# Performance work log

Hardware: AMD Instinct MI355X
Metric: run time of the kernel (lower is better)

Reference implementation:

```python
import jax, jax.numpy as jnp
import numpy as np

NUM_EXPERTS = 8
NUM_LANGS = 4
TOP_K = 2
D_MODEL = 1024
EXPERT_SIZE = 4096
B, S = 2, 2048


def setup_inputs() -> dict:
    key = jax.random.key(0)
    ks = jax.random.split(key, 6)
    def xavier(k, shape, fan_in, fan_out):
        a = float(np.sqrt(6.0 / (fan_in + fan_out)))
        return jax.random.uniform(k, shape, jnp.float32, -a, a)
    return {
        "x": jax.random.normal(ks[0], (B, S, D_MODEL), jnp.float32),
        "router_w": xavier(ks[1], (NUM_EXPERTS, D_MODEL), D_MODEL, NUM_EXPERTS),
        "router_b": jnp.zeros((NUM_EXPERTS,), jnp.float32),
        "lang_w": xavier(ks[2], (NUM_LANGS, D_MODEL), D_MODEL, NUM_LANGS),
        "lang_b": jnp.zeros((NUM_LANGS,), jnp.float32),
        "w1": xavier(ks[3], (NUM_EXPERTS, D_MODEL, EXPERT_SIZE), D_MODEL, EXPERT_SIZE),
        "b1": jnp.zeros((NUM_EXPERTS, EXPERT_SIZE), jnp.float32),
        "w2": xavier(ks[4], (NUM_EXPERTS, EXPERT_SIZE, D_MODEL), EXPERT_SIZE, D_MODEL),
        "b2": jnp.zeros((NUM_EXPERTS, D_MODEL), jnp.float32),
    }


def reference(x, router_w, router_b, lang_w, lang_b, w1, b1, w2, b2):
    # Language-aware routing bias
    lang_logits = x @ lang_w.T + lang_b                      # [B,S,L]
    lang_probs = jax.nn.softmax(lang_logits, axis=-1)
    # lang_probs[..., idx:idx+2].sum(-1): slice may be width 1 at the edge,
    # emulate with a zero pad column.
    lp_pad = jnp.pad(lang_probs, ((0, 0), (0, 0), (0, 1)))
    idx = jnp.arange(NUM_EXPERTS) % NUM_LANGS                # [E]
    expert_weights = lp_pad[..., idx] + lp_pad[..., idx + 1] # [B,S,E]

    router_logits = x @ router_w.T + router_b + 0.1 * expert_weights
    router_probs = jax.nn.softmax(router_logits, axis=-1)   # [B,S,E]
    top_p, top_i = jax.lax.top_k(router_probs, TOP_K)        # [B,S,K]
    top_p = top_p / top_p.sum(axis=-1, keepdims=True)

    # Dense per-expert MLP (dropout=0 / eval). torch GELU default = exact erf.
    h = jax.nn.gelu(jnp.einsum('bsd,edh->bseh', x, w1) + b1, approximate=False)
    expert_out = jnp.einsum('bseh,ehd->bsed', h, w2) + b2    # [B,S,E,D]

    sel = jnp.take_along_axis(expert_out, top_i[..., None], axis=2)  # [B,S,K,D]
    return (top_p[..., None] * sel).sum(axis=2)              # [B,S,D]
```

## Files before the change

### kernel.cpp

```cpp
#include <hip/hip_runtime.h>
#include <cstdint>
#include <cstddef>

#define T_TOK 4096
#define DM 1024
#define HS 4096
#define NE 8
#define MAXROWS 9216
#define MAXTILES 72

typedef __attribute__((ext_vector_type(8))) short short8;
typedef __attribute__((ext_vector_type(4))) float floatx4;

__device__ __forceinline__ unsigned short f2bf(float f) {
  union { float f; unsigned u; } v; v.f = f;
  unsigned r = (v.u + 0x7fffu + ((v.u >> 16) & 1u)) >> 16;
  return (unsigned short)r;
}

__device__ __forceinline__ void gload_lds16(const void* g, void* l) {
  __builtin_amdgcn_global_load_lds((const __attribute__((address_space(1))) void*)g,
                                   (__attribute__((address_space(3))) void*)l, 16, 0, 0);
}


__global__ void k_init(int* counts, int* cursor, unsigned* list) {
  int i = blockIdx.x * 256 + threadIdx.x;
  if (i < NE) { counts[i] = 0; cursor[i] = 0; }
  if (i < MAXROWS) list[i] = 0xFFFFFFFFu;
}

__global__ void k_route(const float* __restrict__ x, const float* __restrict__ rw,
                        const float* __restrict__ rb, const float* __restrict__ lw,
                        const float* __restrict__ lb, int* __restrict__ top_i,
                        float* __restrict__ top_p, int* __restrict__ counts) {
  int t = blockIdx.x * 4 + (threadIdx.x >> 6);
  int lane = threadIdx.x & 63;
  const float4* xt = (const float4*)(x + (size_t)t * DM);
  float4 xv[4];
#pragma unroll
  for (int j = 0; j < 4; j++) xv[j] = xt[lane * 4 + j];
  float dots[12];
#pragma unroll
  for (int r = 0; r < 12; r++) {
    const float4* wr = (const float4*)(r < 4 ? lw + r * DM : rw + (r - 4) * DM);
    float s = 0.f;
#pragma unroll
    for (int j = 0; j < 4; j++) {
      float4 w = wr[lane * 4 + j];
      s += xv[j].x * w.x + xv[j].y * w.y + xv[j].z * w.z + xv[j].w * w.w;
    }
#pragma unroll
    for (int o = 32; o > 0; o >>= 1) s += __shfl_xor(s, o, 64);
    dots[r] = s;
  }
  if (lane == 0) {
    float lp[4]; float m = -1e30f;
#pragma unroll
    for (int i = 0; i < 4; i++) { lp[i] = dots[i] + lb[i]; m = fmaxf(m, lp[i]); }
    float sum = 0.f;
#pragma unroll
    for (int i = 0; i < 4; i++) { lp[i] = expf(lp[i] - m); sum += lp[i]; }
#pragma unroll
    for (int i = 0; i < 4; i++) lp[i] /= sum;
    float ew[4];
    ew[0] = lp[0] + lp[1]; ew[1] = lp[1] + lp[2]; ew[2] = lp[2] + lp[3]; ew[3] = lp[3];
    float r8[8];
#pragma unroll
    for (int e = 0; e < 8; e++) r8[e] = dots[4 + e] + rb[e] + 0.1f * ew[e & 3];
    int e0 = 0;
#pragma unroll
    for (int e = 1; e < 8; e++) if (r8[e] > r8[e0]) e0 = e;
    int e1 = (e0 == 0) ? 1 : 0;
#pragma unroll
    for (int e = 0; e < 8; e++) if (e != e0 && r8[e] > r8[e1]) e1 = e;
    float tt = expf(r8[e1] - r8[e0]);
    float w0 = 1.f / (1.f + tt);
    float w1 = tt / (1.f + tt);
    top_i[t * 2] = e0; top_i[t * 2 + 1] = e1;
    top_p[t * 2] = w0; top_p[t * 2 + 1] = w1;
    atomicAdd(&counts[e0], 1); atomicAdd(&counts[e1], 1);
  }
}

__global__ void k_offsets(const int* counts, int* off) {
  if (threadIdx.x == 0) {
    int acc = 0;
    for (int e = 0; e < NE; e++) {
      off[e] = acc;
      int p = ((counts[e] + 127) >> 7) << 7;
      acc += p;
    }
    off[NE] = acc;
  }
}

__global__ void k_scatter(const int* __restrict__ top_i, const int* __restrict__ off,
                          int* cursor, unsigned* __restrict__ list) {
  int t = blockIdx.x * 256 + threadIdx.x;
  if (t >= T_TOK) return;
#pragma unroll
  for (int k = 0; k < 2; k++) {
    int e = top_i[t * 2 + k];
    int pos = atomicAdd(&cursor[e], 1);
    list[off[e] + pos] = (unsigned)(t * 2 + k);
  }
}

__global__ void k_cvt_x(const float* __restrict__ x, unsigned short* __restrict__ xb) {
  int i = blockIdx.x * 256 + threadIdx.x;
  float4 v = ((const float4*)x)[i];
  union { unsigned short us[4]; uint2 u2; } o;
  o.us[0] = f2bf(v.x); o.us[1] = f2bf(v.y); o.us[2] = f2bf(v.z); o.us[3] = f2bf(v.w);
  ((uint2*)xb)[i] = o.u2;
}

__global__ void k_transpose_bf16(const float* __restrict__ src, unsigned short* __restrict__ dst,
                                 int K, int N) {
  __shared__ float tile[64][65];
  const float* s = src + (size_t)blockIdx.z * K * N;
  unsigned short* d = dst + (size_t)blockIdx.z * K * N;
  int n0 = blockIdx.x * 64, k0 = blockIdx.y * 64;
  int r = threadIdx.x >> 6, c = threadIdx.x & 63;
#pragma unroll
  for (int j = 0; j < 16; j++) tile[r + j * 4][c] = s[(size_t)(k0 + r + j * 4) * N + n0 + c];
  __syncthreads();
#pragma unroll
  for (int j = 0; j < 16; j++) d[(size_t)(n0 + r + j * 4) * K + k0 + c] = f2bf(tile[c][r + j * 4]);
}

__global__ void k_init_out(const int* __restrict__ top_i, const float* __restrict__ top_p,
                           const float* __restrict__ b2, float* __restrict__ out) {
  int i = blockIdx.x * 256 + threadIdx.x;
  int t = i >> 10, d = i & 1023;
  int e0 = top_i[t * 2], e1 = top_i[t * 2 + 1];
  out[i] = top_p[t * 2] * b2[e0 * DM + d] + top_p[t * 2 + 1] * b2[e1 * DM + d];
}

template <int MODE>
__global__ __launch_bounds__(256, 2) void k_gemm(
    const unsigned short* __restrict__ Abase,
    const unsigned short* __restrict__ Wt,
    const int* __restrict__ off, const unsigned* __restrict__ list,
    const float* __restrict__ b1, const float* __restrict__ top_p,
    unsigned short* __restrict__ Hout, float* __restrict__ out,
    int K, int N) {
  int r0 = blockIdx.x * 128;
  int total = off[NE];
  if (r0 >= total) return;
  int e = 0;
  while (r0 >= off[e + 1]) ++e;
  int n0 = blockIdx.y * 128;

  __shared__ __align__(16) unsigned short lA[128 * 32];
  __shared__ __align__(16) unsigned short lB[128 * 32];
  __shared__ float sP[128];
  __shared__ int sTok[128];

  int tid = threadIdx.x;
  int srow = tid >> 2;
  int koff = (tid & 3) * 8;

  const unsigned short* srcA[2];
#pragma unroll
  for (int c = 0; c < 2; c++) {
    int row = c * 64 + srow;
    size_t arow;
    if (MODE == 0) {
      unsigned pair = list[r0 + row];
      arow = (pair == 0xFFFFFFFFu) ? 0 : (size_t)(pair >> 1);
    } else {
      arow = (size_t)(r0 + row);
    }
    srcA[c] = Abase + arow * K + koff;
  }
  const unsigned short* srcB[2];
#pragma unroll
  for (int c = 0; c < 2; c++)
    srcB[c] = Wt + ((size_t)e * N + n0 + c * 64 + srow) * K + koff;

  if (MODE == 1 && tid < 128) {
    unsigned pair = list[r0 + tid];
    if (pair == 0xFFFFFFFFu) { sTok[tid] = -1; sP[tid] = 0.f; }
    else { sTok[tid] = (int)(pair >> 1); sP[tid] = top_p[pair]; }
  }

  floatx4 acc[4][4] = {};
  int lane = tid & 63;
  int w = tid >> 6;
  int wm = w >> 1, wn = w & 1;
  int lr = lane & 15, kq = lane >> 4;
  const short8* pA = (const short8*)lA;
  const short8* pB = (const short8*)lB;

  for (int k0 = 0; k0 < K; k0 += 32) {
    __syncthreads();
#pragma unroll
    for (int c = 0; c < 2; c++) {
      gload_lds16(srcA[c] + k0, &lA[(c * 64 + srow) * 32 + koff]);
      gload_lds16(srcB[c] + k0, &lB[(c * 64 + srow) * 32 + koff]);
    }
    __syncthreads();
    short8 a[4], b[4];
#pragma unroll
    for (int i = 0; i < 4; i++) a[i] = pA[((wm * 64 + i * 16 + lr) * 32 + kq * 8) >> 3];
#pragma unroll
    for (int j = 0; j < 4; j++) b[j] = pB[((wn * 64 + j * 16 + lr) * 32 + kq * 8) >> 3];
#pragma unroll
    for (int i = 0; i < 4; i++)
#pragma unroll
      for (int j = 0; j < 4; j++)
        acc[i][j] = __builtin_amdgcn_mfma_f32_16x16x32_bf16(a[i], b[j], acc[i][j], 0, 0, 0);
  }

  int rbase = wm * 64 + kq * 4;
  int cbase = wn * 64 + lr;
  if (MODE == 0) {
#pragma unroll
    for (int i = 0; i < 4; i++)
#pragma unroll
      for (int j = 0; j < 4; j++)
#pragma unroll
        for (int g = 0; g < 4; g++) {
          int row = rbase + i * 16 + g;
          int col = cbase + j * 16;
          float v = acc[i][j][g] + b1[e * HS + n0 + col];
          v = 0.5f * v * (1.f + erff(v * 0.70710678118f));
          Hout[(size_t)(r0 + row) * (size_t)N + n0 + col] = f2bf(v);
        }
  } else {
#pragma unroll
    for (int i = 0; i < 4; i++)
#pragma unroll
      for (int j = 0; j < 4; j++)
#pragma unroll
        for (int g = 0; g < 4; g++) {
          int row = rbase + i * 16 + g;
          int col = cbase + j * 16;
          int tok = sTok[row];
          if (tok >= 0)
            atomicAdd(&out[(size_t)tok * DM + n0 + col], sP[row] * acc[i][j][g]);
        }
  }
}


extern "C" void kernel_launch(void* const* d_in, const int* in_sizes, int n_in,
                              void* d_out, int out_size, void* d_ws, size_t ws_size,
                              hipStream_t stream) {
  const float* x  = (const float*)d_in[0];
  const float* rw = (const float*)d_in[1];
  const float* rb = (const float*)d_in[2];
  const float* lw = (const float*)d_in[3];
  const float* lb = (const float*)d_in[4];
  const float* w1 = (const float*)d_in[5];
  const float* b1 = (const float*)d_in[6];
  const float* w2 = (const float*)d_in[7];
  const float* b2 = (const float*)d_in[8];
  float* out = (float*)d_out;
  char* ws = (char*)d_ws;

  int* counts = (int*)ws;
  int* cursor = (int*)(ws + 32);
  int* off    = (int*)(ws + 64);
  int* top_i  = (int*)(ws + 128);
  float* top_p = (float*)(ws + 128 + 32768);
  unsigned* list = (unsigned*)(ws + 65792);
  unsigned short* xb = (unsigned short*)(ws + 102912);
  unsigned short* wt = (unsigned short*)(ws + 102912 + 8388608);
  unsigned short* h  = (unsigned short*)(ws + 102912 + 8388608 + 67108864);

  k_init<<<dim3((MAXROWS + 255) / 256), dim3(256), 0, stream>>>(counts, cursor, list);
  k_route<<<dim3(T_TOK / 4), dim3(256), 0, stream>>>(x, rw, rb, lw, lb, top_i, top_p, counts);
  k_offsets<<<dim3(1), dim3(64), 0, stream>>>(counts, off);
  k_scatter<<<dim3(T_TOK / 256), dim3(256), 0, stream>>>(top_i, off, cursor, list);
  k_cvt_x<<<dim3(T_TOK * DM / 4 / 256), dim3(256), 0, stream>>>(x, xb);
  k_transpose_bf16<<<dim3(HS / 64, DM / 64, NE), dim3(256), 0, stream>>>(w1, wt, DM, HS);
  k_gemm<0><<<dim3(MAXTILES, HS / 128), dim3(256), 0, stream>>>(
      xb, wt, off, list, b1, top_p, h, nullptr, DM, HS);
  k_transpose_bf16<<<dim3(DM / 64, HS / 64, NE), dim3(256), 0, stream>>>(w2, wt, HS, DM);
  k_init_out<<<dim3(T_TOK * DM / 256), dim3(256), 0, stream>>>(top_i, top_p, b2, out);
  k_gemm<1><<<dim3(MAXTILES, DM / 128), dim3(256), 0, stream>>>(
      h, wt, off, list, nullptr, top_p, nullptr, out, HS, DM);
}
```

Before: 533.9 us.

## Double-buffer GEMM LDS loads, swizzle LDS layout, remap tiles, vectorize transpose

The GEMM main loop now double-buffers its LDS tiles, issuing the next k-slice load before running the MFMAs on the current one, and needs one barrier per iteration instead of two. The global-to-LDS source offsets are XOR-swizzled by row so that fragment reads avoid LDS bank conflicts. Block indices are remapped with a stride-8 interleave, presumably to spread tiles across XCDs or improve L2 reuse, and the grid is transposed to match. Occupancy hint is raised to 4 blocks per CU. The weight transpose kernel now uses float4 reads and 8-byte bf16 writes. The costs are twice the LDS, added register pressure, and a swizzle formula that assumes the tile count divides by 8.

Measured after the change: 515.4 us. 1.04x faster.

```diff
diff --git a/kernel.cpp b/kernel.cpp
--- a/kernel.cpp
+++ b/kernel.cpp
@@ -121,12 +121,24 @@
   const float* s = src + (size_t)blockIdx.z * K * N;
   unsigned short* d = dst + (size_t)blockIdx.z * K * N;
   int n0 = blockIdx.x * 64, k0 = blockIdx.y * 64;
-  int r = threadIdx.x >> 6, c = threadIdx.x & 63;
-#pragma unroll
-  for (int j = 0; j < 16; j++) tile[r + j * 4][c] = s[(size_t)(k0 + r + j * 4) * N + n0 + c];
+  int tr = threadIdx.x >> 4;
+  int tc = (threadIdx.x & 15) * 4;
+#pragma unroll
+  for (int j = 0; j < 4; j++) {
+    int row = tr + j * 16;
+    float4 v = *(const float4*)&s[(size_t)(k0 + row) * N + n0 + tc];
+    tile[row][tc + 0] = v.x; tile[row][tc + 1] = v.y;
+    tile[row][tc + 2] = v.z; tile[row][tc + 3] = v.w;
+  }
   __syncthreads();
 #pragma unroll
-  for (int j = 0; j < 16; j++) d[(size_t)(n0 + r + j * 4) * K + k0 + c] = f2bf(tile[c][r + j * 4]);
+  for (int j = 0; j < 4; j++) {
+    int n = tr + j * 16;
+    union { unsigned short us[4]; uint2 u2; } o;
+#pragma unroll
+    for (int i = 0; i < 4; i++) o.us[i] = f2bf(tile[tc + i][n]);
+    *(uint2*)&d[(size_t)(n0 + n) * K + k0 + tc] = o.u2;
+  }
 }
 
 __global__ void k_init_out(const int* __restrict__ top_i, const float* __restrict__ top_p,
@@ -138,28 +150,35 @@
 }
 
 template <int MODE>
-__global__ __launch_bounds__(256, 2) void k_gemm(
+__global__ __launch_bounds__(256, 4) void k_gemm(
     const unsigned short* __restrict__ Abase,
     const unsigned short* __restrict__ Wt,
     const int* __restrict__ off, const unsigned* __restrict__ list,
     const float* __restrict__ b1, const float* __restrict__ top_p,
     unsigned short* __restrict__ Hout, float* __restrict__ out,
     int K, int N) {
-  int r0 = blockIdx.x * 128;
+  int nx = gridDim.x;
+  int flat = blockIdx.y * nx + blockIdx.x;
+  int cpx = (nx * gridDim.y) >> 3;
+  int swz = (flat & 7) * cpx + (flat >> 3);
+  int n0 = (swz % nx) * 128;
+  int r0 = (swz / nx) * 128;
+
   int total = off[NE];
   if (r0 >= total) return;
   int e = 0;
   while (r0 >= off[e + 1]) ++e;
-  int n0 = blockIdx.y * 128;
-
-  __shared__ __align__(16) unsigned short lA[128 * 32];
-  __shared__ __align__(16) unsigned short lB[128 * 32];
+
+  __shared__ __align__(16) unsigned short lA[2][128 * 32];
+  __shared__ __align__(16) unsigned short lB[2][128 * 32];
   __shared__ float sP[128];
   __shared__ int sTok[128];
 
   int tid = threadIdx.x;
   int srow = tid >> 2;
-  int koff = (tid & 3) * 8;
+  int key_s = (srow >> 1) & 3;
+  int koff_src = (((tid & 3) ^ key_s) * 8);
+  int kdst = (tid & 3) * 8;
 
   const unsigned short* srcA[2];
 #pragma unroll
@@ -172,12 +191,12 @@
     } else {
       arow = (size_t)(r0 + row);
     }
-    srcA[c] = Abase + arow * K + koff;
+    srcA[c] = Abase + arow * K + koff_src;
   }
   const unsigned short* srcB[2];
 #pragma unroll
   for (int c = 0; c < 2; c++)
-    srcB[c] = Wt + ((size_t)e * N + n0 + c * 64 + srow) * K + koff;
+    srcB[c] = Wt + ((size_t)e * N + n0 + c * 64 + srow) * K + koff_src;
 
   if (MODE == 1 && tid < 128) {
     unsigned pair = list[r0 + tid];
@@ -190,28 +209,39 @@
   int w = tid >> 6;
   int wm = w >> 1, wn = w & 1;
   int lr = lane & 15, kq = lane >> 4;
-  const short8* pA = (const short8*)lA;
-  const short8* pB = (const short8*)lB;
-
+  int kx = kq ^ ((lr >> 1) & 3);
+
+#define STAGE(BUF, KK)                                                        \
+  do {                                                                        \
+    _Pragma("unroll")                                                         \
+    for (int c = 0; c < 2; c++) {                                             \
+      gload_lds16(srcA[c] + (KK), &lA[BUF][(c * 64 + srow) * 32 + kdst]);     \
+      gload_lds16(srcB[c] + (KK), &lB[BUF][(c * 64 + srow) * 32 + kdst]);     \
+    }                                                                         \
+  } while (0)
+
+  STAGE(0, 0);
+  __syncthreads();
+
+  int cur = 0;
   for (int k0 = 0; k0 < K; k0 += 32) {
-    __syncthreads();
-#pragma unroll
-    for (int c = 0; c < 2; c++) {
-      gload_lds16(srcA[c] + k0, &lA[(c * 64 + srow) * 32 + koff]);
-      gload_lds16(srcB[c] + k0, &lB[(c * 64 + srow) * 32 + koff]);
-    }
-    __syncthreads();
+    if (k0 + 32 < K) STAGE(cur ^ 1, k0 + 32);
+    const short8* pA = (const short8*)lA[cur];
+    const short8* pB = (const short8*)lB[cur];
     short8 a[4], b[4];
 #pragma unroll
-    for (int i = 0; i < 4; i++) a[i] = pA[((wm * 64 + i * 16 + lr) * 32 + kq * 8) >> 3];
-#pragma unroll
-    for (int j = 0; j < 4; j++) b[j] = pB[((wn * 64 + j * 16 + lr) * 32 + kq * 8) >> 3];
+    for (int i = 0; i < 4; i++) a[i] = pA[(wm * 64 + i * 16 + lr) * 4 + kx];
+#pragma unroll
+    for (int j = 0; j < 4; j++) b[j] = pB[(wn * 64 + j * 16 + lr) * 4 + kx];
 #pragma unroll
     for (int i = 0; i < 4; i++)
 #pragma unroll
       for (int j = 0; j < 4; j++)
         acc[i][j] = __builtin_amdgcn_mfma_f32_16x16x32_bf16(a[i], b[j], acc[i][j], 0, 0, 0);
-  }
+    __syncthreads();
+    cur ^= 1;
+  }
+#undef STAGE
 
   int rbase = wm * 64 + kq * 4;
   int cbase = wn * 64 + lr;
@@ -276,10 +306,10 @@
   k_scatter<<<dim3(T_TOK / 256), dim3(256), 0, stream>>>(top_i, off, cursor, list);
   k_cvt_x<<<dim3(T_TOK * DM / 4 / 256), dim3(256), 0, stream>>>(x, xb);
   k_transpose_bf16<<<dim3(HS / 64, DM / 64, NE), dim3(256), 0, stream>>>(w1, wt, DM, HS);
-  k_gemm<0><<<dim3(MAXTILES, HS / 128), dim3(256), 0, stream>>>(
+  k_gemm<0><<<dim3(HS / 128, MAXTILES), dim3(256), 0, stream>>>(
       xb, wt, off, list, b1, top_p, h, nullptr, DM, HS);
   k_transpose_bf16<<<dim3(DM / 64, HS / 64, NE), dim3(256), 0, stream>>>(w2, wt, HS, DM);
   k_init_out<<<dim3(T_TOK * DM / 256), dim3(256), 0, stream>>>(top_i, top_p, b2, out);
-  k_gemm<1><<<dim3(MAXTILES, DM / 128), dim3(256), 0, stream>>>(
+  k_gemm<1><<<dim3(DM / 128, MAXTILES), dim3(256), 0, stream>>>(
       h, wt, off, list, nullptr, top_p, nullptr, out, HS, DM);
 }
```
